# Optimization experiments

Measured on AMD Instinct MI355X. Metric: run time of the kernel, lower is better.

## Reference

```python
import jax, jax.numpy as jnp
import numpy as np

T = 4            # timesteps (init arg T)
K = 8            # num_thresholds
B = 64           # batch per timestep (x.shape[0] == T*B)


def setup_inputs() -> dict:
    key = jax.random.key(0)
    kx, = jax.random.split(key, 1)
    x = jax.random.normal(kx, (T * B, 128, 32, 32), dtype=jnp.float32)
    thresh = jnp.asarray(1.0, dtype=jnp.float32)  # scalar learnable threshold
    return {"x": x, "thresh": thresh}


def reference(x, thresh):
    # thre_shaped: thresh / 2**k, shaped [K, 1,1,1,1] to broadcast over mem[None] = [1,B,C,H,W]
    thre = (thresh / (2.0 ** jnp.arange(K, dtype=x.dtype))).reshape((K,) + (1,) * x.ndim)
    thr75 = thre * 0.75

    xt = x.reshape((T, x.shape[0] // T) + x.shape[1:])  # expand: [T, B, C, H, W]

    def step(mem, xc):
        mem = mem + xc
        # which thresholds the membrane exceeds (thresholds are decreasing in k)
        pos = (mem[None] >= thr75).astype(x.dtype)           # [K, B, C, H, W]
        pos_true = pos.at[1:].add(-pos[:-1])                 # first (largest) crossed threshold only
        spike = jnp.sum(thre * pos_true, axis=0)             # [B, C, H, W]
        return mem - spike, spike

    mem0 = jnp.zeros_like(xt[0])
    _, spikes = jax.lax.scan(step, mem0, xt)                 # spikes: [T, B, C, H, W]
    return spikes.reshape(x.shape)                            # merge: [T*B, C, H, W]
```

## Files before the change

kernel.cpp:

```cpp
#include <hip/hip_runtime.h>


constexpr int T_STEPS = 4;
constexpr int K_THRESH = 8;

__global__ __launch_bounds__(256) void snn_mth_kernel(
    const float* __restrict__ x,
    const float* __restrict__ p_thresh,
    float* __restrict__ out,
    int s4)
{
    int i = blockIdx.x * blockDim.x + threadIdx.x;
    if (i >= s4) return;

    const float thresh = *p_thresh;

    float thre[K_THRESH], thr75[K_THRESH];
    {
        float tk = thresh;
        float t75 = 0.75f * thresh;
#pragma unroll
        for (int k = 0; k < K_THRESH; ++k) {
            thre[k] = tk;
            thr75[k] = t75;
            tk *= 0.5f;
            t75 *= 0.5f;
        }
    }

    const float4* __restrict__ xv = reinterpret_cast<const float4*>(x);
    float4* __restrict__ ov = reinterpret_cast<float4*>(out);

    float4 mem = make_float4(0.f, 0.f, 0.f, 0.f);

#pragma unroll
    for (int t = 0; t < T_STEPS; ++t) {
        float4 xc = xv[(size_t)t * s4 + i];
        mem.x += xc.x;
        mem.y += xc.y;
        mem.z += xc.z;
        mem.w += xc.w;

        float4 sp = make_float4(0.f, 0.f, 0.f, 0.f);
#pragma unroll
        for (int k = K_THRESH - 1; k >= 0; --k) {
            sp.x = (mem.x >= thr75[k]) ? thre[k] : sp.x;
            sp.y = (mem.y >= thr75[k]) ? thre[k] : sp.y;
            sp.z = (mem.z >= thr75[k]) ? thre[k] : sp.z;
            sp.w = (mem.w >= thr75[k]) ? thre[k] : sp.w;
        }

        ov[(size_t)t * s4 + i] = sp;

        mem.x -= sp.x;
        mem.y -= sp.y;
        mem.z -= sp.z;
        mem.w -= sp.w;
    }
}

extern "C" void kernel_launch(void* const* d_in, const int* in_sizes, int n_in,
                              void* d_out, int out_size, void* d_ws, size_t ws_size,
                              hipStream_t stream) {
    const float* x = (const float*)d_in[0];
    const float* p_thresh = (const float*)d_in[1];
    float* out = (float*)d_out;

    const int total = in_sizes[0];
    const int S = total / T_STEPS;
    const int s4 = S >> 2;

    const int block = 256;
    const int grid = (s4 + block - 1) / block;
    snn_mth_kernel<<<grid, block, 0, stream>>>(x, p_thresh, out, s4);
}
```

Measured before the change: 234.9 us.

## Use persistent grid with double-buffered loads, bit-trick thresholds, nontemporal stores

Replaces the one-thread-per-element launch with a fixed grid-stride loop that prefetches the next tile's four timestep vectors while computing the current one. The eight-way threshold compare chain is swapped for an integer exponent trick that derives the crossed power-of-two threshold directly from the float bits. Outputs are written with nontemporal stores. The bit trick assumes a positive normal threshold and exact power-of-two spacing, and the fixed grid of 1024 blocks may underfill or overfill the device.

```diff
diff --git a/kernel.cpp b/kernel.cpp
--- a/kernel.cpp
+++ b/kernel.cpp
@@ -2,60 +2,83 @@
 
 
 constexpr int T_STEPS = 4;
-constexpr int K_THRESH = 8;
+constexpr int BLOCK = 256;
+constexpr int GRID = 1024;
 
-__global__ __launch_bounds__(256) void snn_mth_kernel(
+typedef float v4f __attribute__((ext_vector_type(4)));
+
+__device__ __forceinline__ void load4(v4f dst[T_STEPS], const v4f* __restrict__ xv,
+                                      size_t n, size_t j) {
+#pragma unroll
+    for (int t = 0; t < T_STEPS; ++t) dst[t] = xv[(size_t)t * n + j];
+}
+
+__device__ __forceinline__ float spike_of(float mem, int b75_0, int b75_7, int bth0) {
+    int u = __float_as_int(mem);
+    int d = (int)((unsigned)b75_0 - (unsigned)u);
+    int k = (int)((unsigned)d + 0x7fffffu) >> 23;
+    k = k > 0 ? k : 0;
+    int sb = bth0 - (k << 23);
+    return (u >= b75_7) ? __int_as_float(sb) : 0.0f;
+}
+
+__device__ __forceinline__ void process(const v4f a[T_STEPS], v4f* __restrict__ ov,
+                                        size_t n, size_t j,
+                                        int b75_0, int b75_7, int bth0) {
+    v4f sp[T_STEPS];
+#pragma unroll
+    for (int e = 0; e < 4; ++e) {
+        float mem = a[0][e];
+        float s0 = spike_of(mem, b75_0, b75_7, bth0);
+        sp[0][e] = s0;
+        mem = mem - s0 + a[1][e];
+        float s1 = spike_of(mem, b75_0, b75_7, bth0);
+        sp[1][e] = s1;
+        mem = mem - s1 + a[2][e];
+        float s2 = spike_of(mem, b75_0, b75_7, bth0);
+        sp[2][e] = s2;
+        mem = mem - s2 + a[3][e];
+        sp[3][e] = spike_of(mem, b75_0, b75_7, bth0);
+    }
+#pragma unroll
+    for (int t = 0; t < T_STEPS; ++t)
+        __builtin_nontemporal_store(sp[t], &ov[(size_t)t * n + j]);
+}
+
+__global__ __launch_bounds__(BLOCK) void snn_mth_kernel(
     const float* __restrict__ x,
     const float* __restrict__ p_thresh,
     float* __restrict__ out,
     int s4)
 {
-    int i = blockIdx.x * blockDim.x + threadIdx.x;
-    if (i >= s4) return;
+    const float thresh = *p_thresh;
+    const int bth0  = __float_as_int(thresh);
+    const int b75_0 = __float_as_int(0.75f * thresh);
+    const int b75_7 = b75_0 - 7 * 0x800000;
 
-    const float thresh = *p_thresh;
+    const v4f* __restrict__ xv = reinterpret_cast<const v4f*>(x);
+    v4f* __restrict__ ov = reinterpret_cast<v4f*>(out);
 
-    float thre[K_THRESH], thr75[K_THRESH];
-    {
-        float tk = thresh;
-        float t75 = 0.75f * thresh;
-#pragma unroll
-        for (int k = 0; k < K_THRESH; ++k) {
-            thre[k] = tk;
-            thr75[k] = t75;
-            tk *= 0.5f;
-            t75 *= 0.5f;
-        }
-    }
+    const size_t n = (size_t)s4;
+    const size_t stride = (size_t)GRID * BLOCK;
 
-    const float4* __restrict__ xv = reinterpret_cast<const float4*>(x);
-    float4* __restrict__ ov = reinterpret_cast<float4*>(out);
+    size_t jA = (size_t)blockIdx.x * BLOCK + threadIdx.x;
+    v4f A[T_STEPS], B[T_STEPS];
+    bool actA = jA < n;
+    if (actA) load4(A, xv, n, jA);
 
-    float4 mem = make_float4(0.f, 0.f, 0.f, 0.f);
+    while (actA) {
+        size_t jB = jA + stride;
+        bool actB = jB < n;
+        if (actB) load4(B, xv, n, jB);
+        process(A, ov, n, jA, b75_0, b75_7, bth0);
 
-#pragma unroll
-    for (int t = 0; t < T_STEPS; ++t) {
-        float4 xc = xv[(size_t)t * s4 + i];
-        mem.x += xc.x;
-        mem.y += xc.y;
-        mem.z += xc.z;
-        mem.w += xc.w;
-
-        float4 sp = make_float4(0.f, 0.f, 0.f, 0.f);
-#pragma unroll
-        for (int k = K_THRESH - 1; k >= 0; --k) {
-            sp.x = (mem.x >= thr75[k]) ? thre[k] : sp.x;
-            sp.y = (mem.y >= thr75[k]) ? thre[k] : sp.y;
-            sp.z = (mem.z >= thr75[k]) ? thre[k] : sp.z;
-            sp.w = (mem.w >= thr75[k]) ? thre[k] : sp.w;
-        }
-
-        ov[(size_t)t * s4 + i] = sp;
-
-        mem.x -= sp.x;
-        mem.y -= sp.y;
-        mem.z -= sp.z;
-        mem.w -= sp.w;
+        size_t jA2 = jB + stride;
+        actA = jA2 < n;
+        if (actA) load4(A, xv, n, jA2);
+        if (!actB) break;
+        process(B, ov, n, jB, b75_0, b75_7, bth0);
+        jA = jA2;
     }
 }
 
@@ -70,7 +93,5 @@
     const int S = total / T_STEPS;
     const int s4 = S >> 2;
 
-    const int block = 256;
-    const int grid = (s4 + block - 1) / block;
-    snn_mth_kernel<<<grid, block, 0, stream>>>(x, p_thresh, out, s4);
+    snn_mth_kernel<<<GRID, BLOCK, 0, stream>>>(x, p_thresh, out, s4);
 }
```

After: 246.7 us. 1.05x slower.
